# Kernel tuning notes

Measured on AMD Instinct MI355X. Metric: run time of the kernel, lower is better.

The kernel has to match this reference:

```python
import jax, jax.numpy as jnp
import numpy as np

IN_FEATURES = 512
OUT_FEATURES = 256
BATCH = 1024


def setup_inputs() -> dict:
    key = jax.random.key(0)
    k1, k2, k3, k4 = jax.random.split(key, 4)
    n_lower = IN_FEATURES * (IN_FEATURES - 1) // 2  # strictly-lower triangle count
    return {
        "inputs": jax.random.normal(k1, (BATCH, IN_FEATURES), dtype=jnp.float32),
        "weight": jax.random.normal(k2, (OUT_FEATURES, 1, IN_FEATURES), dtype=jnp.float32),
        "L_diags": jax.random.uniform(k3, (OUT_FEATURES, IN_FEATURES), dtype=jnp.float32),
        "L_lower": jax.random.normal(k4, (OUT_FEATURES, n_lower), dtype=jnp.float32) * 0.05,
    }


def _build_L(L_diags, L_lower):
    # Per-class lower-triangular matrix: diag = L_diags**2, strict lower = L_lower.
    K, d = L_diags.shape
    ri, ci = np.tril_indices(d, k=-1)  # static index pattern (row-major, matches torch.tril_indices)
    diag_idx = jnp.arange(d)
    L = jnp.zeros((K, d, d), dtype=L_diags.dtype)
    L = L.at[:, diag_idx, diag_idx].set(jnp.square(L_diags))
    L = L.at[:, ri, ci].set(L_lower)
    return L  # [K, d, d]


def reference(inputs, weight, L_diags, L_lower):
    L = _build_L(L_diags, L_lower)                      # [K, d, d]
    pinputs = jnp.einsum('bd,kde->kbe', inputs, L)      # [K, B, d]
    pweights = jnp.einsum('kod,kde->koe', weight, L)    # [K, 1, d]
    dist = pinputs - pweights                           # broadcast over B -> [K, B, d]
    out = jnp.sqrt(jnp.sum(jnp.square(dist), axis=2))   # torch.norm(dim=2) -> [K, B]
    return out.T                                        # [B, K]
```

## Files before the change

kernel.cpp:

```cpp
#include <hip/hip_runtime.h>
#include <hip/hip_bf16.h>
#include <math.h>

#define B_SZ   1024
#define D_SZ   512
#define KC_SZ  256
#define NLOW   130816

#define STEP_ELEMS  8192
#define NSTEPS      20
#define CLASS_ELEMS (NSTEPS * STEP_ELEMS)

#define OFF_XP     (size_t)(KC_SZ * CLASS_ELEMS * 2)
#define OFF_TPART  (OFF_XP + 64 * STEP_ELEMS * 2)
#define OFF_T      (OFF_TPART + (size_t)KC_SZ * 8 * 512 * 4)
#define WS_NEED    (OFF_T + (size_t)KC_SZ * 512 * 4)

typedef __attribute__((ext_vector_type(4))) float  f32x4;
typedef __attribute__((ext_vector_type(4), aligned(4))) float f32x4u;
typedef __attribute__((ext_vector_type(8))) __bf16 bf16x8;

__device__ __forceinline__ int sbase_of(int ct) { return ct * (9 - ct); }
__device__ __forceinline__ int kch_of(int s) {
    return (s < 8) ? s : (s < 14) ? s - 6 : (s < 18) ? s - 10 : s - 12;
}

__global__ __launch_bounds__(256)
void prep_all(const float* __restrict__ X,
              const float* __restrict__ Ldiag,
              const float* __restrict__ Llow,
              const float* __restrict__ W,
              __hip_bfloat16* __restrict__ Xp,
              __hip_bfloat16* __restrict__ Bp,
              float* __restrict__ tpart) {
    __shared__ __bf16 Lt[128 * 64];
    __shared__ float  ptl[32 * 129];

    const int bx  = blockIdx.x;
    const int tid = threadIdx.x;

    if (bx < 64) {
        const int pg  = bx;
        const int mt  = pg >> 3, kch = pg & 7;
        __bf16* out = (__bf16*)Xp + (size_t)pg * STEP_ELEMS;
        #pragma unroll
        for (int i = 0; i < 4; ++i) {
            const int line = tid + i * 256;
            const int wmg = line >> 9, mi = (line >> 7) & 3, h = (line >> 6) & 1;
            const int lane = line & 63, q = lane >> 4, c = lane & 15;
            const int row = mt * 128 + wmg * 64 + mi * 16 + c;
            const float* src = X + (size_t)row * D_SZ + kch * 64 + h * 32 + q * 8;
            f32x4 v0 = ((const f32x4*)src)[0];
            f32x4 v1 = ((const f32x4*)src)[1];
            bf16x8 p;
            #pragma unroll
            for (int j = 0; j < 4; ++j) { p[j] = (__bf16)v0[j]; p[j + 4] = (__bf16)v1[j]; }
            *(bf16x8*)(out + line * 8) = p;
        }
        return;
    }

    const int idx = bx - 64;
    const int s   = idx % 20;
    const int kc  = idx / 20;
    const int ct = (s < 8) ? 0 : (s < 14) ? 1 : (s < 18) ? 2 : 3;
    const int dt = kch_of(s);
    const int e0 = ct << 7, d0 = dt << 6;
    const bool zpage = (dt == 2 * ct);

    const int m   = tid & 31;
    const int seg = tid >> 5;
    const int es  = seg << 4;
    const int dg0 = d0 + 2 * m;

    int cls;
    if (dt >= 2 * ct + 2)      cls = 0;
    else if (dt == 2 * ct + 1) cls = (seg < 4) ? 0 : 1;
    else                       cls = (seg < 4) ? 1 : 2;

    const float* lowb = Llow + (size_t)kc * NLOW;
    const float2 wv = *(const float2*)(W + (size_t)kc * D_SZ + dg0);

    float v0[16], v1[16];
    if (cls == 0) {
        const int t0 = (dg0 * (dg0 - 1)) >> 1;
        const int t1 = t0 + dg0;
        const float* s0 = lowb + t0 + e0 + es;
        const float* s1 = lowb + t1 + e0 + es;
        #pragma unroll
        for (int i = 0; i < 4; ++i) {
            f32x4u a = ((const f32x4u*)s0)[i];
            f32x4u b = ((const f32x4u*)s1)[i];
            #pragma unroll
            for (int j = 0; j < 4; ++j) { v0[i * 4 + j] = a[j]; v1[i * 4 + j] = b[j]; }
        }
    } else if (cls == 1) {
        const int t0 = (dg0 * (dg0 - 1)) >> 1;
        const int t1 = t0 + dg0;
        const float* diagb = Ldiag + (size_t)kc * D_SZ;
        float q0 = diagb[dg0],     q1 = diagb[dg0 + 1];
        q0 *= q0; q1 *= q1;
        #pragma unroll
        for (int j = 0; j < 16; ++j) {
            const int eg = e0 + es + j;
            v0[j] = (eg < dg0)     ? lowb[t0 + eg] : ((eg == dg0)     ? q0 : 0.f);
            v1[j] = (eg < dg0 + 1) ? lowb[t1 + eg] : ((eg == dg0 + 1) ? q1 : 0.f);
        }
    } else {
        #pragma unroll
        for (int j = 0; j < 16; ++j) { v0[j] = 0.f; v1[j] = 0.f; }
    }

    char* ltb = (char*)Lt;
    #pragma unroll
    for (int j = 0; j < 16; ++j) {
        const int el = es + j;
        union { __bf16 h[2]; unsigned u; } pk;
        pk.h[0] = (__bf16)v0[j];
        pk.h[1] = (__bf16)v1[j];
        const int off = el * 128 + ((4 * m) ^ ((el & 7) << 4));
        *(unsigned*)(ltb + off) = pk.u;
        ptl[m * 129 + el] = wv.x * v0[j] + wv.y * v1[j];
    }
    __syncthreads();

    __bf16* page = (__bf16*)Bp + (size_t)kc * CLASS_ELEMS + (size_t)s * STEP_ELEMS;
    const int lane = tid & 63, q = lane >> 4, c = lane & 15;
    #pragma unroll
    for (int k = 0; k < 4; ++k) {
        if (zpage && k >= 2) continue;
        const int ln = k * 256 + tid;
        const int up = ln >> 6;
        const int h  = up & 1;
        const int el = ((up >> 3) << 6) + (((up >> 1) & 3) << 4) + c;
        const int off = el * 128 + (((h << 6) + (q << 4)) ^ ((el & 7) << 4));
        *(bf16x8*)(page + (size_t)ln * 8) = *(const bf16x8*)(ltb + off);
    }

    if (tid < 128) {
        float sum = 0.f;
        #pragma unroll
        for (int mm = 0; mm < 32; ++mm) sum += ptl[mm * 129 + tid];
        tpart[((size_t)(kc * 8 + dt)) * 512 + e0 + tid] = sum;
    }
}

__global__ __launch_bounds__(256, 2)
void gml2_main(const __hip_bfloat16* __restrict__ Xp,
               const __hip_bfloat16* __restrict__ Bp,
               const float* __restrict__ tpart,
               float* __restrict__ Out) {
    __shared__ __align__(16) char ldsbuf[2][32768];
    __shared__ float tvs[512];

    const int tid = threadIdx.x;
    const int bx  = blockIdx.x;
    const int xcd = bx & 7;
    const int g   = bx >> 3;
    const int kc  = xcd * 32 + (g >> 3);
    const int mt  = g & 7;

    const int lane = tid & 63;
    const int wave = tid >> 6;
    const int wmg  = wave & 1;
    const int wng  = wave >> 1;
    const int c    = lane & 15;
    const int q    = lane >> 4;

    const __bf16* pA = (const __bf16*)Xp + (size_t)(mt * 8) * STEP_ELEMS;
    const __bf16* pB = (const __bf16*)Bp + (size_t)kc * CLASS_ELEMS;

    int aoff[4][2], boff[4][2];
    #pragma unroll
    for (int mi = 0; mi < 4; ++mi)
        #pragma unroll
        for (int h = 0; h < 2; ++h)
            aoff[mi][h] = (((wmg * 4 + mi) * 2 + h) * 64 + lane) * 16;
    #pragma unroll
    for (int ni = 0; ni < 4; ++ni)
        #pragma unroll
        for (int h = 0; h < 2; ++h)
            boff[ni][h] = (((wng * 4 + ni) * 2 + h) * 64 + lane) * 16;

    f32x4 acc[4][4];
    #pragma unroll
    for (int mi = 0; mi < 4; ++mi)
        #pragma unroll
        for (int ni = 0; ni < 4; ++ni)
            acc[mi][ni] = (f32x4){0.f, 0.f, 0.f, 0.f};
    float rsum[16];
    #pragma unroll
    for (int i = 0; i < 16; ++i) rsum[i] = 0.f;

#define STAGE(BUF, SIDX, NB) {                                                 \
    const int kch_ = kch_of(SIDX);                                             \
    const char* ga_ = (const char*)(pA + (size_t)kch_ * STEP_ELEMS);           \
    const char* gb_ = (const char*)(pB + (size_t)(SIDX) * STEP_ELEMS);         \
    char* la_ = &ldsbuf[BUF][0];                                               \
    char* lb_ = &ldsbuf[BUF][16384];                                           \
    _Pragma("unroll") for (int i_ = 0; i_ < 4; ++i_) {                         \
        const int ch_ = (wave * 4 + i_) * 1024;                                \
        __builtin_amdgcn_global_load_lds(                                      \
            (const __attribute__((address_space(1))) void*)(ga_ + ch_ + lane * 16), \
            (__attribute__((address_space(3))) void*)(la_ + ch_), 16, 0, 0);   \
    }                                                                          \
    _Pragma("unroll") for (int i_ = 0; i_ < (NB); ++i_) {                      \
        const int ch_ = (wave * (NB) + i_) * 1024;                             \
        __builtin_amdgcn_global_load_lds(                                      \
            (const __attribute__((address_space(1))) void*)(gb_ + ch_ + lane * 16), \
            (__attribute__((address_space(3))) void*)(lb_ + ch_), 16, 0, 0);   \
    } }

#define WAIT8 asm volatile("s_waitcnt vmcnt(8)" ::: "memory")
#define WAIT6 asm volatile("s_waitcnt vmcnt(6)" ::: "memory")
#define WAIT0 asm volatile("s_waitcnt vmcnt(0)" ::: "memory")

#define GSTEP(S, ZS, NBN, WMAC) {                                              \
    if ((S) + 1 < NSTEPS) STAGE(((S) + 1) & 1, (S) + 1, NBN);                  \
    WMAC;                                                                      \
    __builtin_amdgcn_s_barrier();                                              \
    if (!(ZS) || wng == 0) {                                                   \
        const char* la_ = &ldsbuf[(S) & 1][0];                                 \
        const char* lb_ = &ldsbuf[(S) & 1][16384];                             \
        bf16x8 fa[4][2], fb[4][2];                                             \
        _Pragma("unroll") for (int mi = 0; mi < 4; ++mi)                       \
        _Pragma("unroll") for (int h = 0; h < 2; ++h)                          \
            fa[mi][h] = *(const bf16x8*)(la_ + aoff[mi][h]);                   \
        _Pragma("unroll") for (int ni = 0; ni < 4; ++ni)                       \
        _Pragma("unroll") for (int h = 0; h < 2; ++h)                          \
            fb[ni][h] = *(const bf16x8*)(lb_ + boff[ni][h]);                   \
        _Pragma("unroll") for (int h = 0; h < 2; ++h)                          \
        _Pragma("unroll") for (int mi = 0; mi < 4; ++mi)                       \
        _Pragma("unroll") for (int ni = 0; ni < 4; ++ni)                       \
            acc[mi][ni] = __builtin_amdgcn_mfma_f32_16x16x32_bf16(             \
                fa[mi][h], fb[ni][h], acc[mi][ni], 0, 0, 0);                   \
    }                                                                          \
    __builtin_amdgcn_s_barrier(); }

#define FOLD(CT) {                                                             \
    float tv_[4];                                                              \
    _Pragma("unroll") for (int ni = 0; ni < 4; ++ni)                           \
        tv_[ni] = tvs[(CT) * 128 + wng * 64 + ni * 16 + c];                    \
    _Pragma("unroll") for (int mi = 0; mi < 4; ++mi)                           \
    _Pragma("unroll") for (int ni = 0; ni < 4; ++ni)                           \
    _Pragma("unroll") for (int r = 0; r < 4; ++r) {                            \
        float y_ = acc[mi][ni][r] - tv_[ni];                                   \
        rsum[mi * 4 + r] += y_ * y_;                                           \
        acc[mi][ni][r] = 0.f; } }

    STAGE(0, 0, 2);

    if (tid < 128) {
        const int ctq = tid >> 5;
        f32x4 ssum = (f32x4){0.f, 0.f, 0.f, 0.f};
        for (int dt = ctq << 1; dt < 8; ++dt)
            ssum += ((const f32x4*)(tpart + ((size_t)(kc * 8 + dt)) * 512))[tid];
        ((f32x4*)tvs)[tid] = ssum;
    }
    __syncthreads();

    GSTEP(0, 1, 4, WAIT8) GSTEP(1, 0, 4, WAIT8) GSTEP(2, 0, 4, WAIT8)
    GSTEP(3, 0, 4, WAIT8) GSTEP(4, 0, 4, WAIT8) GSTEP(5, 0, 4, WAIT8)
    GSTEP(6, 0, 4, WAIT8) GSTEP(7, 0, 2, WAIT6)
    FOLD(0)
    GSTEP(8, 1, 4, WAIT8) GSTEP(9, 0, 4, WAIT8) GSTEP(10, 0, 4, WAIT8)
    GSTEP(11, 0, 4, WAIT8) GSTEP(12, 0, 4, WAIT8) GSTEP(13, 0, 2, WAIT6)
    FOLD(1)
    GSTEP(14, 1, 4, WAIT8) GSTEP(15, 0, 4, WAIT8) GSTEP(16, 0, 4, WAIT8)
    GSTEP(17, 0, 2, WAIT6)
    FOLD(2)
    GSTEP(18, 1, 4, WAIT8) GSTEP(19, 0, 4, WAIT0)
    FOLD(3)

    #pragma unroll
    for (int i = 0; i < 16; ++i) {
        float v = rsum[i];
        v += __shfl_xor(v, 1, 64);
        v += __shfl_xor(v, 2, 64);
        v += __shfl_xor(v, 4, 64);
        v += __shfl_xor(v, 8, 64);
        rsum[i] = v;
    }
    float (*osum)[128] = (float(*)[128])&ldsbuf[0][0];
    if (c == 0) {
        #pragma unroll
        for (int mi = 0; mi < 4; ++mi)
            #pragma unroll
            for (int r = 0; r < 4; ++r)
                osum[wng][wmg * 64 + mi * 16 + q * 4 + r] = rsum[mi * 4 + r];
    }
    __syncthreads();
    if (tid < 128) {
        float v = osum[0][tid] + osum[1][tid];
        Out[(size_t)(mt * 128 + tid) * KC_SZ + kc] = sqrtf(v);
    }
}

#define FLDA 40
#define BM 128
#define BN 128
__device__ __forceinline__ void fstep_map(int s, int& ct, int& k0) {
    if (s < 16)      { ct = 0; k0 = s * 32; }
    else if (s < 28) { ct = 1; k0 = 128 + (s - 16) * 32; }
    else if (s < 36) { ct = 2; k0 = 256 + (s - 28) * 32; }
    else             { ct = 3; k0 = 384 + (s - 36) * 32; }
}
__global__ __launch_bounds__(256, 2)
void gml2_fallback(const float* __restrict__ X, const float* __restrict__ W,
                   const float* __restrict__ Ldiag, const float* __restrict__ Llow,
                   float* __restrict__ Out) {
    __shared__ __bf16 As[BM * FLDA];
    __shared__ __bf16 Bs[BN * FLDA];
    __shared__ float  Ws[D_SZ];
    __shared__ float  osum[2][BM];
    const int tid = threadIdx.x;
    const int bx  = blockIdx.x;
    const int xcd = bx & 7;
    const int g   = bx >> 3;
    const int kc  = xcd * 32 + (g >> 3);
    const int mt  = g & 7;
    const int lane = tid & 63, wave = tid >> 6;
    const int wm = (wave & 1) * 64, wn = (wave >> 1) * 64;
    const int c = lane & 15, q = lane >> 4;
    const int am = tid >> 1, akh = (tid & 1) << 4;
    const float* xrow = X + (size_t)(mt * BM + am) * D_SZ;
    const float* wrow = W + (size_t)kc * D_SZ;
    const int be = tid & 127, bd = (tid >> 7) << 4;
    const float* lowbase  = Llow  + (size_t)kc * NLOW;
    const float* diagbase = Ldiag + (size_t)kc * D_SZ;
    if (tid < 128) ((f32x4*)Ws)[tid] = ((const f32x4*)wrow)[tid];
    float rsum[16];
    #pragma unroll
    for (int i = 0; i < 16; ++i) rsum[i] = 0.f;
    f32x4 acc[4][4];
    #pragma unroll
    for (int mi = 0; mi < 4; ++mi)
        #pragma unroll
        for (int ni = 0; ni < 4; ++ni) acc[mi][ni] = (f32x4){0.f, 0.f, 0.f, 0.f};
    f32x4 xr[4];
    float bb[16];
    auto prefetch = [&](int s) {
        int pct, pk0; fstep_map(s, pct, pk0);
        const int pe0 = pct * BN;
        const float* xp = xrow + pk0 + akh;
        #pragma unroll
        for (int i = 0; i < 4; ++i) xr[i] = ((const f32x4*)xp)[i];
        const int e = pe0 + be, d0 = pk0 + bd;
        int tri = (d0 * (d0 - 1)) >> 1;
        if (pk0 >= pe0 + BN) {
            #pragma unroll
            for (int j = 0; j < 16; ++j) { bb[j] = lowbase[tri + e]; tri += d0 + j; }
        } else {
            #pragma unroll
            for (int j = 0; j < 16; ++j) {
                const int d = d0 + j;
                float val = 0.f;
                if (d > e)       val = lowbase[tri + e];
                else if (d == e) { float dq = diagbase[d]; val = dq * dq; }
                bb[j] = val; tri += d;
            }
        }
    };
    prefetch(0);
    __syncthreads();
    int cur_ct = 0;
    for (int s = 0; s < 40; ++s) {
        int ct, k0; fstep_map(s, ct, k0);
        if (ct != cur_ct) {
            #pragma unroll
            for (int mi = 0; mi < 4; ++mi)
                #pragma unroll
                for (int ni = 0; ni < 4; ++ni)
                    #pragma unroll
                    for (int r = 0; r < 4; ++r) {
                        float y = acc[mi][ni][r];
                        rsum[mi * 4 + r] += y * y;
                        acc[mi][ni][r] = 0.f;
                    }
            cur_ct = ct;
        }
        bf16x8 ap0, ap1;
        {
            const f32x4* wsp = (const f32x4*)&Ws[k0 + akh];
            #pragma unroll
            for (int i = 0; i < 4; ++i) {
                f32x4 wv = wsp[i];
                #pragma unroll
                for (int l = 0; l < 4; ++l) {
                    float v = xr[i][l] - wv[l];
                    int idx = i * 4 + l;
                    if (idx < 8) ap0[idx] = (__bf16)v;
                    else         ap1[idx - 8] = (__bf16)v;
                }
            }
        }
        bf16x8 bp0, bp1;
        #pragma unroll
        for (int j = 0; j < 8; ++j) { bp0[j] = (__bf16)bb[j]; bp1[j] = (__bf16)bb[j + 8]; }
        __syncthreads();
        *(bf16x8*)&As[am * FLDA + akh]     = ap0;
        *(bf16x8*)&As[am * FLDA + akh + 8] = ap1;
        *(bf16x8*)&Bs[be * FLDA + bd]      = bp0;
        *(bf16x8*)&Bs[be * FLDA + bd + 8]  = bp1;
        if (s + 1 < 40) prefetch(s + 1);
        __syncthreads();
        bf16x8 af[4], bfr[4];
        #pragma unroll
        for (int mi = 0; mi < 4; ++mi)
            af[mi] = *(const bf16x8*)&As[(wm + mi * 16 + c) * FLDA + q * 8];
        #pragma unroll
        for (int ni = 0; ni < 4; ++ni)
            bfr[ni] = *(const bf16x8*)&Bs[(wn + ni * 16 + c) * FLDA + q * 8];
        #pragma unroll
        for (int mi = 0; mi < 4; ++mi)
            #pragma unroll
            for (int ni = 0; ni < 4; ++ni)
                acc[mi][ni] = __builtin_amdgcn_mfma_f32_16x16x32_bf16(
                    af[mi], bfr[ni], acc[mi][ni], 0, 0, 0);
    }
    #pragma unroll
    for (int mi = 0; mi < 4; ++mi)
        #pragma unroll
        for (int ni = 0; ni < 4; ++ni)
            #pragma unroll
            for (int r = 0; r < 4; ++r) {
                float y = acc[mi][ni][r];
                rsum[mi * 4 + r] += y * y;
            }
    #pragma unroll
    for (int i = 0; i < 16; ++i) {
        float s = rsum[i];
        s += __shfl_xor(s, 1, 64);
        s += __shfl_xor(s, 2, 64);
        s += __shfl_xor(s, 4, 64);
        s += __shfl_xor(s, 8, 64);
        rsum[i] = s;
    }
    const int wnIdx = wave >> 1;
    if (c == 0) {
        #pragma unroll
        for (int mi = 0; mi < 4; ++mi)
            #pragma unroll
            for (int r = 0; r < 4; ++r)
                osum[wnIdx][wm + mi * 16 + q * 4 + r] = rsum[mi * 4 + r];
    }
    __syncthreads();
    if (tid < BM) {
        float s = osum[0][tid] + osum[1][tid];
        Out[(size_t)(mt * BM + tid) * KC_SZ + kc] = sqrtf(s);
    }
}

extern "C" void kernel_launch(void* const* d_in, const int* in_sizes, int n_in,
                              void* d_out, int out_size, void* d_ws, size_t ws_size,
                              hipStream_t stream) {
    const float* X  = (const float*)d_in[0];
    const float* W  = (const float*)d_in[1];
    const float* Ld = (const float*)d_in[2];
    const float* Ll = (const float*)d_in[3];
    float* Out = (float*)d_out;

    if (ws_size >= WS_NEED) {
        __hip_bfloat16* Bp    = (__hip_bfloat16*)d_ws;
        __hip_bfloat16* Xp    = (__hip_bfloat16*)((char*)d_ws + OFF_XP);
        float*          tpart = (float*)((char*)d_ws + OFF_TPART);
        prep_all<<<dim3(64 + NSTEPS * KC_SZ), dim3(256), 0, stream>>>(
            X, Ld, Ll, W, Xp, Bp, tpart);
        gml2_main<<<dim3(KC_SZ * 8), dim3(256), 0, stream>>>(Xp, Bp, tpart, Out);
    } else {
        gml2_fallback<<<dim3(KC_SZ * 8), dim3(256), 0, stream>>>(X, W, Ld, Ll, Out);
    }
}
```

Baseline: 347.0 us.

## Load B fragments directly to registers, double-buffer them, and reduce T in separate kernel

The main GEMM kernel now reads the per-class L fragments straight from global memory into double-buffered registers instead of staging them through LDS. LDS now holds only the A tile, so the LDS footprint is halved and occupancy may rise. The per-class T vector reduction moves into a new small kernel, and each thread loads its T values into registers up front. The prep kernel now writes the zero half-pages too, and the zero-skip that let some waves skip MFMAs on diagonal steps is removed, so those steps do extra work. The register pressure from the B double buffer and the extra launch are the main risks.

```diff
diff --git a/kernel.cpp b/kernel.cpp
--- a/kernel.cpp
+++ b/kernel.cpp
@@ -66,7 +66,6 @@
     const int ct = (s < 8) ? 0 : (s < 14) ? 1 : (s < 18) ? 2 : 3;
     const int dt = kch_of(s);
     const int e0 = ct << 7, d0 = dt << 6;
-    const bool zpage = (dt == 2 * ct);
 
     const int m   = tid & 31;
     const int seg = tid >> 5;
@@ -128,7 +127,6 @@
     const int lane = tid & 63, q = lane >> 4, c = lane & 15;
     #pragma unroll
     for (int k = 0; k < 4; ++k) {
-        if (zpage && k >= 2) continue;
         const int ln = k * 256 + tid;
         const int up = ln >> 6;
         const int h  = up & 1;
@@ -145,13 +143,24 @@
     }
 }
 
+__global__ __launch_bounds__(256)
+void t_reduce(const float* __restrict__ tpart, float* __restrict__ Tv) {
+    const int idx = blockIdx.x * 256 + threadIdx.x;
+    const int kc = idx >> 9, e = idx & 511;
+    const int ct = e >> 7;
+    float s = 0.f;
+    for (int dt = ct << 1; dt < 8; ++dt)
+        s += tpart[((size_t)(kc * 8 + dt)) * 512 + e];
+    Tv[idx] = s;
+}
+
 __global__ __launch_bounds__(256, 2)
 void gml2_main(const __hip_bfloat16* __restrict__ Xp,
                const __hip_bfloat16* __restrict__ Bp,
-               const float* __restrict__ tpart,
+               const float* __restrict__ Tv,
                float* __restrict__ Out) {
-    __shared__ __align__(16) char ldsbuf[2][32768];
-    __shared__ float tvs[512];
+    __shared__ __align__(16) char abuf[2][16384];
+    __shared__ float osum[2][128];
 
     const int tid = threadIdx.x;
     const int bx  = blockIdx.x;
@@ -170,17 +179,25 @@
     const __bf16* pA = (const __bf16*)Xp + (size_t)(mt * 8) * STEP_ELEMS;
     const __bf16* pB = (const __bf16*)Bp + (size_t)kc * CLASS_ELEMS;
 
-    int aoff[4][2], boff[4][2];
+    float tvr[4][4];
+    #pragma unroll
+    for (int ct4 = 0; ct4 < 4; ++ct4)
+        #pragma unroll
+        for (int ni = 0; ni < 4; ++ni)
+            tvr[ct4][ni] = Tv[kc * 512 + ct4 * 128 + wng * 64 + ni * 16 + c];
+
+    int aoff[4][2];
     #pragma unroll
     for (int mi = 0; mi < 4; ++mi)
         #pragma unroll
         for (int h = 0; h < 2; ++h)
             aoff[mi][h] = (((wmg * 4 + mi) * 2 + h) * 64 + lane) * 16;
+    int boff[4][2];
     #pragma unroll
     for (int ni = 0; ni < 4; ++ni)
         #pragma unroll
         for (int h = 0; h < 2; ++h)
-            boff[ni][h] = (((wng * 4 + ni) * 2 + h) * 64 + lane) * 16;
+            boff[ni][h] = ((((wng * 4 + ni) * 2 + h) * 64) + lane) * 8;
 
     f32x4 acc[4][4];
     #pragma unroll
@@ -192,84 +209,69 @@
     #pragma unroll
     for (int i = 0; i < 16; ++i) rsum[i] = 0.f;
 
-#define STAGE(BUF, SIDX, NB) {                                                 \
+    bf16x8 fbA[4][2], fbB[4][2];
+
+#define STAGE_A(BUF, SIDX) {                                                   \
     const int kch_ = kch_of(SIDX);                                             \
     const char* ga_ = (const char*)(pA + (size_t)kch_ * STEP_ELEMS);           \
-    const char* gb_ = (const char*)(pB + (size_t)(SIDX) * STEP_ELEMS);         \
-    char* la_ = &ldsbuf[BUF][0];                                               \
-    char* lb_ = &ldsbuf[BUF][16384];                                           \
+    char* la_ = &abuf[BUF][0];                                                 \
     _Pragma("unroll") for (int i_ = 0; i_ < 4; ++i_) {                         \
         const int ch_ = (wave * 4 + i_) * 1024;                                \
         __builtin_amdgcn_global_load_lds(                                      \
             (const __attribute__((address_space(1))) void*)(ga_ + ch_ + lane * 16), \
             (__attribute__((address_space(3))) void*)(la_ + ch_), 16, 0, 0);   \
+    } }
+
+#define LOAD_B(FB, SP) { const __bf16* p_ = pB + (size_t)(SP) * STEP_ELEMS;    \
+    _Pragma("unroll") for (int ni = 0; ni < 4; ++ni)                           \
+    _Pragma("unroll") for (int h = 0; h < 2; ++h)                              \
+        FB[ni][h] = *(const bf16x8*)(p_ + boff[ni][h]); }
+
+#define FOLD(CT) {                                                             \
+    _Pragma("unroll") for (int mi = 0; mi < 4; ++mi)                           \
+    _Pragma("unroll") for (int ni = 0; ni < 4; ++ni)                           \
+    _Pragma("unroll") for (int r = 0; r < 4; ++r) {                            \
+        float y_ = acc[mi][ni][r] - tvr[CT][ni];                               \
+        rsum[mi * 4 + r] += y_ * y_;                                           \
+        acc[mi][ni][r] = 0.f; } }
+
+#define GSTEP(S, FBC, FBN) {                                                   \
+    if ((S) + 1 < NSTEPS) {                                                    \
+        LOAD_B(FBN, (S) + 1);                                                  \
+        STAGE_A(((S) + 1) & 1, (S) + 1);                                       \
+        asm volatile("s_waitcnt vmcnt(12)" ::: "memory");                      \
+    } else {                                                                   \
+        asm volatile("s_waitcnt vmcnt(0)" ::: "memory");                       \
     }                                                                          \
-    _Pragma("unroll") for (int i_ = 0; i_ < (NB); ++i_) {                      \
-        const int ch_ = (wave * (NB) + i_) * 1024;                             \
-        __builtin_amdgcn_global_load_lds(                                      \
-            (const __attribute__((address_space(1))) void*)(gb_ + ch_ + lane * 16), \
-            (__attribute__((address_space(3))) void*)(lb_ + ch_), 16, 0, 0);   \
-    } }
-
-#define WAIT8 asm volatile("s_waitcnt vmcnt(8)" ::: "memory")
-#define WAIT6 asm volatile("s_waitcnt vmcnt(6)" ::: "memory")
-#define WAIT0 asm volatile("s_waitcnt vmcnt(0)" ::: "memory")
-
-#define GSTEP(S, ZS, NBN, WMAC) {                                              \
-    if ((S) + 1 < NSTEPS) STAGE(((S) + 1) & 1, (S) + 1, NBN);                  \
-    WMAC;                                                                      \
-    __builtin_amdgcn_s_barrier();                                              \
-    if (!(ZS) || wng == 0) {                                                   \
-        const char* la_ = &ldsbuf[(S) & 1][0];                                 \
-        const char* lb_ = &ldsbuf[(S) & 1][16384];                             \
-        bf16x8 fa[4][2], fb[4][2];                                             \
+    __builtin_amdgcn_s_barrier();          \
+    {                                                                          \
+        const char* la_ = &abuf[(S) & 1][0];                                   \
+        bf16x8 fa[4][2];                                                       \
         _Pragma("unroll") for (int mi = 0; mi < 4; ++mi)                       \
         _Pragma("unroll") for (int h = 0; h < 2; ++h)                          \
             fa[mi][h] = *(const bf16x8*)(la_ + aoff[mi][h]);                   \
-        _Pragma("unroll") for (int ni = 0; ni < 4; ++ni)                       \
-        _Pragma("unroll") for (int h = 0; h < 2; ++h)                          \
-            fb[ni][h] = *(const bf16x8*)(lb_ + boff[ni][h]);                   \
         _Pragma("unroll") for (int h = 0; h < 2; ++h)                          \
         _Pragma("unroll") for (int mi = 0; mi < 4; ++mi)                       \
         _Pragma("unroll") for (int ni = 0; ni < 4; ++ni)                       \
             acc[mi][ni] = __builtin_amdgcn_mfma_f32_16x16x32_bf16(             \
-                fa[mi][h], fb[ni][h], acc[mi][ni], 0, 0, 0);                   \
+                fa[mi][h], FBC[ni][h], acc[mi][ni], 0, 0, 0);                  \
     }                                                                          \
     __builtin_amdgcn_s_barrier(); }
 
-#define FOLD(CT) {                                                             \
-    float tv_[4];                                                              \
-    _Pragma("unroll") for (int ni = 0; ni < 4; ++ni)                           \
-        tv_[ni] = tvs[(CT) * 128 + wng * 64 + ni * 16 + c];                    \
-    _Pragma("unroll") for (int mi = 0; mi < 4; ++mi)                           \
-    _Pragma("unroll") for (int ni = 0; ni < 4; ++ni)                           \
-    _Pragma("unroll") for (int r = 0; r < 4; ++r) {                            \
-        float y_ = acc[mi][ni][r] - tv_[ni];                                   \
-        rsum[mi * 4 + r] += y_ * y_;                                           \
-        acc[mi][ni][r] = 0.f; } }
-
-    STAGE(0, 0, 2);
-
-    if (tid < 128) {
-        const int ctq = tid >> 5;
-        f32x4 ssum = (f32x4){0.f, 0.f, 0.f, 0.f};
-        for (int dt = ctq << 1; dt < 8; ++dt)
-            ssum += ((const f32x4*)(tpart + ((size_t)(kc * 8 + dt)) * 512))[tid];
-        ((f32x4*)tvs)[tid] = ssum;
-    }
-    __syncthreads();
-
-    GSTEP(0, 1, 4, WAIT8) GSTEP(1, 0, 4, WAIT8) GSTEP(2, 0, 4, WAIT8)
-    GSTEP(3, 0, 4, WAIT8) GSTEP(4, 0, 4, WAIT8) GSTEP(5, 0, 4, WAIT8)
-    GSTEP(6, 0, 4, WAIT8) GSTEP(7, 0, 2, WAIT6)
+    STAGE_A(0, 0);
+    LOAD_B(fbA, 0);
+
+    GSTEP(0,  fbA, fbB) GSTEP(1,  fbB, fbA) GSTEP(2,  fbA, fbB)
+    GSTEP(3,  fbB, fbA) GSTEP(4,  fbA, fbB) GSTEP(5,  fbB, fbA)
+    GSTEP(6,  fbA, fbB) GSTEP(7,  fbB, fbA)
     FOLD(0)
-    GSTEP(8, 1, 4, WAIT8) GSTEP(9, 0, 4, WAIT8) GSTEP(10, 0, 4, WAIT8)
-    GSTEP(11, 0, 4, WAIT8) GSTEP(12, 0, 4, WAIT8) GSTEP(13, 0, 2, WAIT6)
+    GSTEP(8,  fbA, fbB) GSTEP(9,  fbB, fbA) GSTEP(10, fbA, fbB)
+    GSTEP(11, fbB, fbA) GSTEP(12, fbA, fbB) GSTEP(13, fbB, fbA)
     FOLD(1)
-    GSTEP(14, 1, 4, WAIT8) GSTEP(15, 0, 4, WAIT8) GSTEP(16, 0, 4, WAIT8)
-    GSTEP(17, 0, 2, WAIT6)
+    GSTEP(14, fbA, fbB) GSTEP(15, fbB, fbA) GSTEP(16, fbA, fbB)
+    GSTEP(17, fbB, fbA)
     FOLD(2)
-    GSTEP(18, 1, 4, WAIT8) GSTEP(19, 0, 4, WAIT0)
+    GSTEP(18, fbA, fbB) GSTEP(19, fbB, fbA)
     FOLD(3)
 
     #pragma unroll
@@ -281,7 +283,6 @@
         v += __shfl_xor(v, 8, 64);
         rsum[i] = v;
     }
-    float (*osum)[128] = (float(*)[128])&ldsbuf[0][0];
     if (c == 0) {
         #pragma unroll
         for (int mi = 0; mi < 4; ++mi)
@@ -464,9 +465,11 @@
         __hip_bfloat16* Bp    = (__hip_bfloat16*)d_ws;
         __hip_bfloat16* Xp    = (__hip_bfloat16*)((char*)d_ws + OFF_XP);
         float*          tpart = (float*)((char*)d_ws + OFF_TPART);
+        float*          Tvv   = (float*)((char*)d_ws + OFF_T);
         prep_all<<<dim3(64 + NSTEPS * KC_SZ), dim3(256), 0, stream>>>(
             X, Ld, Ll, W, Xp, Bp, tpart);
-        gml2_main<<<dim3(KC_SZ * 8), dim3(256), 0, stream>>>(Xp, Bp, tpart, Out);
+        t_reduce<<<dim3(512),        dim3(256), 0, stream>>>(tpart, Tvv);
+        gml2_main<<<dim3(KC_SZ * 8), dim3(256), 0, stream>>>(Xp, Bp, Tvv, Out);
     } else {
         gml2_fallback<<<dim3(KC_SZ * 8), dim3(256), 0, stream>>>(X, W, Ld, Ll, Out);
     }
```

Result: slower. 404.3 us (+16.5%).
